# Kernel tuning notes

Hardware: AMD Instinct MI355X
Metric: run time of the kernel (lower is better)

Reference implementation:

```python
import jax, jax.numpy as jnp
import numpy as np

LN_EPS = 1e-5

def _layernorm(x, g, b):
    mu = jnp.mean(x, axis=-1, keepdims=True)
    var = jnp.var(x, axis=-1, keepdims=True)
    return (x - mu) * jax.lax.rsqrt(var + LN_EPS) * g + b

def setup_inputs() -> dict:
    key = jax.random.key(0)
    ks = jax.random.split(key, 8)
    B, N, n, m, a = 4096, 50000, 1024, 16384, 256
    return {
        "x": jax.random.normal(ks[0], (B, n), dtype=jnp.float32),
        "X_data": jax.random.normal(ks[1], (N, n), dtype=jnp.float32),
        "memory_indices": jax.random.randint(ks[2], (m,), 0, N, dtype=jnp.int64)
            if jax.config.jax_enable_x64 else jax.random.randint(ks[2], (m,), 0, N, dtype=jnp.int32),
        "W_q": jax.random.normal(ks[3], (a, n), dtype=jnp.float32) / np.sqrt(n),
        "W_k": jax.random.normal(ks[4], (a, n), dtype=jnp.float32) / np.sqrt(n),
        "W_v": jax.random.normal(ks[5], (n, n), dtype=jnp.float32) / np.sqrt(n),
        "g_q": jnp.ones((a,), jnp.float32), "b_q": jnp.zeros((a,), jnp.float32),
        "g_k": jnp.ones((a,), jnp.float32), "b_k": jnp.zeros((a,), jnp.float32),
        "g_v": jnp.ones((n,), jnp.float32), "b_v": jnp.zeros((n,), jnp.float32),
    }

def reference(x, X_data, memory_indices, W_q, W_k, W_v, g_q, b_q, g_k, b_k, g_v, b_v):
    # Gather memory bank rows: [m, n]
    X_cross = X_data[memory_indices]
    n = x.shape[-1]
    # preprocess(): scalar normalizer so mean row norm ~= sqrt(n) (SAE convention)
    C = jnp.mean(jnp.linalg.norm(X_cross, axis=-1)) / jnp.sqrt(jnp.asarray(n, x.dtype))
    X_cross = X_cross / C
    xs = x / C
    # QKV projections (Linear, no bias) + per-stream LayerNorm
    q = _layernorm(xs @ W_q.T, g_q, b_q)        # [B, a]
    k = _layernorm(X_cross @ W_k.T, g_k, b_k)   # [m, a]
    v = _layernorm(X_cross @ W_v.T, g_v, b_v)   # [m, n]
    # scaled dot-product attention over the memory bank
    scale = 1.0 / np.sqrt(q.shape[-1])
    attn = jax.nn.softmax(jnp.einsum('ba,ma->bm', q, k) * scale, axis=-1)  # [B, m]
    x_hat = attn @ v                             # [B, n]
    return (xs, x_hat, attn, v)
```

## Files before the change

kernel.cpp:

```cpp
#include <hip/hip_runtime.h>
#include <math.h>

typedef _Float16 hlf4 __attribute__((ext_vector_type(4)));
typedef _Float16 hlf8 __attribute__((ext_vector_type(8)));
typedef float f32x4 __attribute__((ext_vector_type(4)));

static __device__ __forceinline__ void gl_lds16(const void* g, void* l) {
    __builtin_amdgcn_global_load_lds(
        (const __attribute__((address_space(1))) unsigned int*)g,
        (__attribute__((address_space(3))) unsigned int*)l, 16, 0, 0);
}

static __device__ __forceinline__ float blk_sum(float v) {
    __shared__ float sm[256];
    int tid = threadIdx.x;
    sm[tid] = v; __syncthreads();
#pragma unroll
    for (int s = 128; s > 0; s >>= 1) {
        if (tid < s) sm[tid] += sm[tid + s];
        __syncthreads();
    }
    float r = sm[0]; __syncthreads();
    return r;
}

static __device__ __forceinline__ float blk_max(float v) {
    __shared__ float sm[256];
    int tid = threadIdx.x;
    sm[tid] = v; __syncthreads();
#pragma unroll
    for (int s = 128; s > 0; s >>= 1) {
        if (tid < s) sm[tid] = fmaxf(sm[tid], sm[tid + s]);
        __syncthreads();
    }
    float r = sm[0]; __syncthreads();
    return r;
}

__global__ __launch_bounds__(256) void k_row_norms(
    const float* __restrict__ X, const int* __restrict__ idx,
    float* __restrict__ norms, int n) {
    long long r = idx[blockIdx.x];
    const float* xr = X + r * (long long)n;
    float s = 0.f;
    for (int k = threadIdx.x * 4; k < n; k += 256 * 4) {
        float4 v = *(const float4*)(xr + k);
        s = fmaf(v.x, v.x, s); s = fmaf(v.y, v.y, s);
        s = fmaf(v.z, v.z, s); s = fmaf(v.w, v.w, s);
    }
    float tot = blk_sum(s);
    if (threadIdx.x == 0) norms[blockIdx.x] = sqrtf(tot);
}

__global__ __launch_bounds__(256) void k_cinv(
    const float* __restrict__ norms, int m, int n, float* __restrict__ cinv) {
    float s = 0.f;
    for (int i = threadIdx.x; i < m; i += 256) s += norms[i];
    float tot = blk_sum(s);
    if (threadIdx.x == 0) cinv[0] = (float)m * sqrtf((float)n) / tot;
}

__global__ __launch_bounds__(256) void k_scale2(
    const float* __restrict__ x, const float* __restrict__ cinv,
    float* __restrict__ y, _Float16* __restrict__ yh, long long total4) {
    float c = cinv[0];
    long long i = blockIdx.x * 256ll + threadIdx.x;
    long long stride = (long long)gridDim.x * 256ll;
    for (; i < total4; i += stride) {
        float4 v = ((const float4*)x)[i];
        v.x *= c; v.y *= c; v.z *= c; v.w *= c;
        ((float4*)y)[i] = v;
        hlf4 o = {(_Float16)v.x, (_Float16)v.y, (_Float16)v.z, (_Float16)v.w};
        ((hlf4*)yh)[i] = o;
    }
}

__global__ __launch_bounds__(256) void k_gather_cvt(
    const float* __restrict__ X, const int* __restrict__ idx,
    const float* __restrict__ cinv, _Float16* __restrict__ out, int n) {
    long long r = idx[blockIdx.x];
    float c = cinv[0];
    const float* src = X + r * (long long)n;
    _Float16* dst = out + (long long)blockIdx.x * n;
    for (int k = threadIdx.x * 4; k < n; k += 256 * 4) {
        float4 v = *(const float4*)(src + k);
        hlf4 o = {(_Float16)(v.x * c), (_Float16)(v.y * c),
                  (_Float16)(v.z * c), (_Float16)(v.w * c)};
        *(hlf4*)(dst + k) = o;
    }
}

__global__ __launch_bounds__(256) void k_cvt(
    const float* __restrict__ in, _Float16* __restrict__ out, long long n4) {
    long long i = blockIdx.x * 256ll + threadIdx.x;
    long long stride = (long long)gridDim.x * 256ll;
    for (; i < n4; i += stride) {
        float4 v = ((const float4*)in)[i];
        hlf4 o = {(_Float16)v.x, (_Float16)v.y, (_Float16)v.z, (_Float16)v.w};
        ((hlf4*)out)[i] = o;
    }
}

__global__ __launch_bounds__(256) void k_tcvt(
    const float* __restrict__ in, _Float16* __restrict__ out, int R, int Cc) {
    __shared__ _Float16 t[32][34];
    int tx = threadIdx.x & 31, ty = threadIdx.x >> 5;
    int c0 = blockIdx.x * 32, r0 = blockIdx.y * 32;
#pragma unroll
    for (int i = 0; i < 32; i += 8)
        t[ty + i][tx] = (_Float16)in[(long long)(r0 + ty + i) * Cc + c0 + tx];
    __syncthreads();
#pragma unroll
    for (int i = 0; i < 32; i += 8)
        out[(long long)(c0 + ty + i) * R + r0 + tx] = t[tx][ty + i];
}

__global__ __launch_bounds__(256) void k_gemm4(
    const _Float16* __restrict__ A, int lda,
    const _Float16* __restrict__ B, int ldb,
    float* __restrict__ Cc, long long ldc, int K,
    float* __restrict__ part, long long zstride) {
    __shared__ _Float16 Ah[2][4096];
    __shared__ _Float16 Bh[2][4096];
    const int tid = threadIdx.x;
    const long long m0 = (long long)blockIdx.x * 128;
    const long long n0 = (long long)blockIdx.y * 128;
    const int KC = K / gridDim.z;
    const int kbase = blockIdx.z * KC;
    const int lane = tid & 63, wv = tid >> 6;
    const int wm = (wv >> 1) * 64, wn = (wv & 1) * 64;
    const int fr = lane & 15, fq = lane >> 4;

    const int s0 = tid, s1 = tid + 256;
    const int r0s = s0 >> 2, r1s = s1 >> 2;
    const int g0 = (((s0 & 3) ^ (r0s & 3)) << 3);
    const int g1 = (((s1 & 3) ^ (r1s & 3)) << 3);
    const _Float16* A0 = A + (m0 + r0s) * (long long)lda + kbase + g0;
    const _Float16* A1 = A + (m0 + r1s) * (long long)lda + kbase + g1;
    const _Float16* B0 = B + (n0 + r0s) * (long long)ldb + kbase + g0;
    const _Float16* B1 = B + (n0 + r1s) * (long long)ldb + kbase + g1;

    f32x4 acc[4][4] = {};

    const int NT = KC / 32;
    {
        gl_lds16(A0, &Ah[0][wv * 512]);
        gl_lds16(A1, &Ah[0][2048 + wv * 512]);
        gl_lds16(B0, &Bh[0][wv * 512]);
        gl_lds16(B1, &Bh[0][2048 + wv * 512]);
    }
    __syncthreads();

    for (int kt = 0; kt < NT; ++kt) {
        const int cur = kt & 1;
        if (kt + 1 < NT) {
            const int nx = cur ^ 1;
            const long long ko = (long long)(kt + 1) * 32;
            gl_lds16(A0 + ko, &Ah[nx][wv * 512]);
            gl_lds16(A1 + ko, &Ah[nx][2048 + wv * 512]);
            gl_lds16(B0 + ko, &Bh[nx][wv * 512]);
            gl_lds16(B1 + ko, &Bh[nx][2048 + wv * 512]);
        }
        hlf8 af[4], bf[4];
#pragma unroll
        for (int i = 0; i < 4; ++i) {
            const int r = wm + i * 16 + fr;
            af[i] = *(const hlf8*)&Ah[cur][r * 32 + ((fq ^ (r & 3)) << 3)];
        }
#pragma unroll
        for (int j = 0; j < 4; ++j) {
            const int r = wn + j * 16 + fr;
            bf[j] = *(const hlf8*)&Bh[cur][r * 32 + ((fq ^ (r & 3)) << 3)];
        }
#pragma unroll
        for (int i = 0; i < 4; ++i)
#pragma unroll
            for (int j = 0; j < 4; ++j)
                acc[i][j] = __builtin_amdgcn_mfma_f32_16x16x32_f16(af[i], bf[j], acc[i][j], 0, 0, 0);
        __syncthreads();
    }

    float* outp = (gridDim.z == 1) ? Cc : (part + (long long)blockIdx.z * zstride);
#pragma unroll
    for (int i = 0; i < 4; ++i)
#pragma unroll
        for (int j = 0; j < 4; ++j) {
            float* cp = outp + (m0 + wm + i * 16 + fq * 4) * ldc + (n0 + wn + j * 16 + fr);
#pragma unroll
            for (int r = 0; r < 4; ++r) cp[(long long)r * ldc] = acc[i][j][r];
        }
}

__global__ __launch_bounds__(512, 2) void k_g256(
    const _Float16* __restrict__ A, int lda,
    const _Float16* __restrict__ B, int ldb,
    float* __restrict__ Cc, long long ldc, int K,
    float* __restrict__ part, long long zstride) {
    __shared__ _Float16 Ah[2][16384];
    __shared__ _Float16 Bh[2][16384];
    const int tid = threadIdx.x, lane = tid & 63, wv = tid >> 6;

    const int gx = gridDim.x, gy = gridDim.y;
    int lin = blockIdx.x + gx * (blockIdx.y + gy * blockIdx.z);
    const int cpx = (gx * gy * (int)gridDim.z) >> 3;
    lin = (lin & 7) * cpx + (lin >> 3);
    const int bx = lin % gx; const int rest = lin / gx;
    const int by = rest % gy, bz = rest / gy;

    const long long m0 = (long long)bx * 256;
    const long long n0 = (long long)by * 256;
    const int KC = K / gridDim.z;
    const int kbase = bz * KC;
    const int wm = (wv >> 2) * 128, wn = (wv & 3) * 64;
    const int fr = lane & 15, fq = lane >> 4;

    const _Float16* srcA[4];
    const _Float16* srcB[4];
#pragma unroll
    for (int j = 0; j < 4; ++j) {
        const int s = j * 512 + tid;
        const int r = s >> 3, p = s & 7;
        const int g = (p ^ (r & 7)) << 3;
        srcA[j] = A + (m0 + r) * (long long)lda + kbase + g;
        srcB[j] = B + (n0 + r) * (long long)ldb + kbase + g;
    }

    f32x4 acc[8][4] = {};

#define ISSUE8(bufi, kt)                                                      \
    {                                                                         \
        const long long ko_ = (long long)(kt) * 64;                           \
        _Float16* la_ = &Ah[bufi][0];                                         \
        _Float16* lb_ = &Bh[bufi][0];                                         \
        gl_lds16(srcA[0] + ko_, la_ + (0 * 512 + wv * 64) * 8);               \
        gl_lds16(srcB[0] + ko_, lb_ + (0 * 512 + wv * 64) * 8);               \
        gl_lds16(srcA[1] + ko_, la_ + (1 * 512 + wv * 64) * 8);               \
        gl_lds16(srcB[1] + ko_, lb_ + (1 * 512 + wv * 64) * 8);               \
        gl_lds16(srcA[2] + ko_, la_ + (2 * 512 + wv * 64) * 8);               \
        gl_lds16(srcB[2] + ko_, lb_ + (2 * 512 + wv * 64) * 8);               \
        gl_lds16(srcA[3] + ko_, la_ + (3 * 512 + wv * 64) * 8);               \
        gl_lds16(srcB[3] + ko_, lb_ + (3 * 512 + wv * 64) * 8);               \
    }

    const int NT = KC / 64;
    ISSUE8(0, 0);
    asm volatile("s_waitcnt vmcnt(0)" ::: "memory");
    __builtin_amdgcn_s_barrier();

    for (int kt = 0; kt < NT; ++kt) {
        const int cur = kt & 1;
        __builtin_amdgcn_s_barrier();
        if (kt + 1 < NT) {
            ISSUE8(cur ^ 1, kt + 1);
            asm volatile("s_waitcnt vmcnt(8)" ::: "memory");
        } else {
            asm volatile("s_waitcnt vmcnt(0)" ::: "memory");
        }
        __builtin_amdgcn_s_barrier();
        __builtin_amdgcn_sched_barrier(0);

        hlf8 af[4][2], bf01[2][2], bf23[2][2];
#pragma unroll
        for (int i = 0; i < 4; ++i)
#pragma unroll
            for (int ks = 0; ks < 2; ++ks) {
                const int rr = wm + i * 16 + fr;
                af[i][ks] = *(const hlf8*)&Ah[cur][rr * 64 + ((((ks * 4 + fq)) ^ (rr & 7)) << 3)];
            }
#pragma unroll
        for (int jj = 0; jj < 2; ++jj)
#pragma unroll
            for (int ks = 0; ks < 2; ++ks) {
                const int cc = wn + jj * 16 + fr;
                bf01[jj][ks] = *(const hlf8*)&Bh[cur][cc * 64 + ((((ks * 4 + fq)) ^ (cc & 7)) << 3)];
            }
        asm volatile("s_waitcnt lgkmcnt(0)" ::: "memory");
        __builtin_amdgcn_sched_barrier(0);
        __builtin_amdgcn_s_setprio(1);
#pragma unroll
        for (int i = 0; i < 4; ++i)
#pragma unroll
            for (int jj = 0; jj < 2; ++jj)
#pragma unroll
                for (int ks = 0; ks < 2; ++ks)
                    acc[i][jj] = __builtin_amdgcn_mfma_f32_16x16x32_f16(af[i][ks], bf01[jj][ks], acc[i][jj], 0, 0, 0);
        __builtin_amdgcn_s_setprio(0);

#pragma unroll
        for (int jj = 0; jj < 2; ++jj)
#pragma unroll
            for (int ks = 0; ks < 2; ++ks) {
                const int cc = wn + (jj + 2) * 16 + fr;
                bf23[jj][ks] = *(const hlf8*)&Bh[cur][cc * 64 + ((((ks * 4 + fq)) ^ (cc & 7)) << 3)];
            }
        asm volatile("s_waitcnt lgkmcnt(0)" ::: "memory");
        __builtin_amdgcn_sched_barrier(0);
        __builtin_amdgcn_s_setprio(1);
#pragma unroll
        for (int i = 0; i < 4; ++i)
#pragma unroll
            for (int jj = 0; jj < 2; ++jj)
#pragma unroll
                for (int ks = 0; ks < 2; ++ks)
                    acc[i][jj + 2] = __builtin_amdgcn_mfma_f32_16x16x32_f16(af[i][ks], bf23[jj][ks], acc[i][jj + 2], 0, 0, 0);
        __builtin_amdgcn_s_setprio(0);

#pragma unroll
        for (int i = 0; i < 4; ++i)
#pragma unroll
            for (int ks = 0; ks < 2; ++ks) {
                const int rr = wm + (i + 4) * 16 + fr;
                af[i][ks] = *(const hlf8*)&Ah[cur][rr * 64 + ((((ks * 4 + fq)) ^ (rr & 7)) << 3)];
            }
        asm volatile("s_waitcnt lgkmcnt(0)" ::: "memory");
        __builtin_amdgcn_sched_barrier(0);
        __builtin_amdgcn_s_setprio(1);
#pragma unroll
        for (int i = 0; i < 4; ++i)
#pragma unroll
            for (int jj = 0; jj < 2; ++jj)
#pragma unroll
                for (int ks = 0; ks < 2; ++ks)
                    acc[i + 4][jj] = __builtin_amdgcn_mfma_f32_16x16x32_f16(af[i][ks], bf01[jj][ks], acc[i + 4][jj], 0, 0, 0);
        __builtin_amdgcn_s_setprio(0);

        __builtin_amdgcn_s_setprio(1);
#pragma unroll
        for (int i = 0; i < 4; ++i)
#pragma unroll
            for (int jj = 0; jj < 2; ++jj)
#pragma unroll
                for (int ks = 0; ks < 2; ++ks)
                    acc[i + 4][jj + 2] = __builtin_amdgcn_mfma_f32_16x16x32_f16(af[i][ks], bf23[jj][ks], acc[i + 4][jj + 2], 0, 0, 0);
        __builtin_amdgcn_s_setprio(0);
    }
#undef ISSUE8

    float* outp = (gridDim.z == 1) ? Cc : (part + (long long)bz * zstride);
#pragma unroll
    for (int i = 0; i < 8; ++i)
#pragma unroll
        for (int j = 0; j < 4; ++j) {
            float* cp = outp + (m0 + wm + i * 16 + fq * 4) * ldc + (n0 + wn + j * 16 + fr);
#pragma unroll
            for (int r = 0; r < 4; ++r) cp[(long long)r * ldc] = acc[i][j][r];
        }
}

__global__ __launch_bounds__(256) void k_redux(
    const float* __restrict__ part, float* __restrict__ out,
    long long n4, long long zs4, int Z) {
    long long i = blockIdx.x * 256ll + threadIdx.x;
    long long stride = (long long)gridDim.x * 256ll;
    for (; i < n4; i += stride) {
        float4 s = ((const float4*)part)[i];
        for (int z = 1; z < Z; ++z) {
            float4 t = ((const float4*)part)[i + z * zs4];
            s.x += t.x; s.y += t.y; s.z += t.z; s.w += t.w;
        }
        ((float4*)out)[i] = s;
    }
}

template <int CNT>
__global__ __launch_bounds__(256) void k_layernorm(
    float* __restrict__ Y, const float* __restrict__ g,
    const float* __restrict__ b, int W) {
    float* yr = Y + (long long)blockIdx.x * W;
    float v[CNT];
    float s = 0.f;
#pragma unroll
    for (int i = 0; i < CNT; ++i) {
        v[i] = yr[threadIdx.x + (i << 8)];
        s += v[i];
    }
    float mu = blk_sum(s) / (float)W;
    float sq = 0.f;
#pragma unroll
    for (int i = 0; i < CNT; ++i) {
        float d = v[i] - mu;
        sq = fmaf(d, d, sq);
    }
    float var = blk_sum(sq) / (float)W;
    float rs = rsqrtf(var + 1e-5f);
#pragma unroll
    for (int i = 0; i < CNT; ++i) {
        int col = threadIdx.x + (i << 8);
        yr[col] = (v[i] - mu) * rs * g[col] + b[col];
    }
}

__global__ __launch_bounds__(256) void k_softmax(
    float* __restrict__ S, _Float16* __restrict__ Sh, float scale) {
    float* sr = S + (long long)blockIdx.x * 16384;
    _Float16* shr = Sh ? Sh + (long long)blockIdx.x * 16384 : nullptr;
    float4 r[16];
    float mx = -1e30f;
#pragma unroll
    for (int i = 0; i < 16; ++i) {
        float4 t = ((const float4*)sr)[threadIdx.x + (i << 8)];
        t.x *= scale; t.y *= scale; t.z *= scale; t.w *= scale;
        r[i] = t;
        mx = fmaxf(mx, fmaxf(fmaxf(t.x, t.y), fmaxf(t.z, t.w)));
    }
    mx = blk_max(mx);
    float sum = 0.f;
#pragma unroll
    for (int i = 0; i < 16; ++i) {
        float4 t = r[i];
        t.x = __expf(t.x - mx); t.y = __expf(t.y - mx);
        t.z = __expf(t.z - mx); t.w = __expf(t.w - mx);
        r[i] = t;
        sum += t.x + t.y + t.z + t.w;
    }
    sum = blk_sum(sum);
    float inv = 1.0f / sum;
#pragma unroll
    for (int i = 0; i < 16; ++i) {
        float4 t = r[i];
        t.x *= inv; t.y *= inv; t.z *= inv; t.w *= inv;
        ((float4*)sr)[threadIdx.x + (i << 8)] = t;
        if (shr) {
            hlf4 o = {(_Float16)t.x, (_Float16)t.y, (_Float16)t.z, (_Float16)t.w};
            ((hlf4*)shr)[threadIdx.x + (i << 8)] = o;
        }
    }
}

extern "C" void kernel_launch(void* const* d_in, const int* in_sizes, int n_in,
                              void* d_out, int out_size, void* d_ws, size_t ws_size,
                              hipStream_t stream) {
    const float* x      = (const float*)d_in[0];
    const float* X_data = (const float*)d_in[1];
    const int*   midx   = (const int*)d_in[2];
    const float* W_q    = (const float*)d_in[3];
    const float* W_k    = (const float*)d_in[4];
    const float* W_v    = (const float*)d_in[5];
    const float* g_q    = (const float*)d_in[6];
    const float* b_q    = (const float*)d_in[7];
    const float* g_k    = (const float*)d_in[8];
    const float* b_k    = (const float*)d_in[9];
    const float* g_v    = (const float*)d_in[10];
    const float* b_v    = (const float*)d_in[11];

    const int n  = in_sizes[10];
    const int a  = in_sizes[6];
    const int m  = in_sizes[2];
    const int Bn = in_sizes[0] / n;

    float* out  = (float*)d_out;
    float* xs   = out;
    float* xhat = xs + (long long)Bn * n;
    float* attn = xhat + (long long)Bn * n;
    float* vout = attn + (long long)Bn * m;

    char* wp = (char*)d_ws;
    auto carve = [&](size_t bytes) -> char* {
        char* r = wp; wp += (bytes + 255) & ~(size_t)255; return r;
    };
    float*     norms = (float*)carve((size_t)m * 4);
    float*     cinv  = (float*)carve(16);
    char*      alias0 = wp;
    float*     qmat  = (float*)carve((size_t)Bn * a * 4);
    float*     kmat  = (float*)carve((size_t)m * a * 4);
    _Float16*  xs_h  = (_Float16*)carve((size_t)Bn * n * 2);
    _Float16*  Xc_h  = (_Float16*)carve((size_t)m * n * 2);
    _Float16*  Wq_h  = (_Float16*)carve((size_t)a * n * 2);
    _Float16*  Wk_h  = (_Float16*)carve((size_t)a * n * 2);
    _Float16*  Wv_h  = (_Float16*)carve((size_t)n * n * 2);
    _Float16*  q_h   = (_Float16*)carve((size_t)Bn * a * 2);
    _Float16*  k_h   = (_Float16*)carve((size_t)m * a * 2);
    float*     splitk = (float*)alias0;
    const int  SK = 4;
    _Float16*  vT_h  = (_Float16*)carve((size_t)n * m * 2);
    size_t used = (size_t)(wp - (char*)d_ws);
    _Float16* attn_h = nullptr;
    if (ws_size >= used + (size_t)Bn * m * 2 + 256)
        attn_h = (_Float16*)carve((size_t)Bn * m * 2);

    hipLaunchKernelGGL(k_row_norms, dim3(m), dim3(256), 0, stream, X_data, midx, norms, n);
    hipLaunchKernelGGL(k_cinv, dim3(1), dim3(256), 0, stream, norms, m, n, cinv);

    hipLaunchKernelGGL(k_scale2, dim3(2048), dim3(256), 0, stream,
                       x, cinv, xs, xs_h, (long long)Bn * n / 4);
    hipLaunchKernelGGL(k_gather_cvt, dim3(m), dim3(256), 0, stream,
                       X_data, midx, cinv, Xc_h, n);

    hipLaunchKernelGGL(k_cvt, dim3(256), dim3(256), 0, stream, W_q, Wq_h, (long long)a * n / 4);
    hipLaunchKernelGGL(k_cvt, dim3(256), dim3(256), 0, stream, W_k, Wk_h, (long long)a * n / 4);
    hipLaunchKernelGGL(k_cvt, dim3(1024), dim3(256), 0, stream, W_v, Wv_h, (long long)n * n / 4);

    hipLaunchKernelGGL(k_gemm4, dim3(Bn / 128, a / 128), dim3(256), 0, stream,
                       xs_h, n, Wq_h, n, qmat, a, n, (float*)nullptr, 0ll);
    hipLaunchKernelGGL(k_gemm4, dim3(m / 128, a / 128), dim3(256), 0, stream,
                       Xc_h, n, Wk_h, n, kmat, a, n, (float*)nullptr, 0ll);
    hipLaunchKernelGGL(k_g256, dim3(m / 256, n / 256), dim3(512), 0, stream,
                       Xc_h, n, Wv_h, n, vout, n, n, (float*)nullptr, 0ll);

    hipLaunchKernelGGL(k_layernorm<1>, dim3(Bn), dim3(256), 0, stream, qmat, g_q, b_q, a);
    hipLaunchKernelGGL(k_layernorm<1>, dim3(m),  dim3(256), 0, stream, kmat, g_k, b_k, a);
    hipLaunchKernelGGL(k_layernorm<4>, dim3(m),  dim3(256), 0, stream, vout, g_v, b_v, n);
    hipLaunchKernelGGL(k_cvt, dim3(1024), dim3(256), 0, stream, qmat, q_h, (long long)Bn * a / 4);
    hipLaunchKernelGGL(k_cvt, dim3(4096), dim3(256), 0, stream, kmat, k_h, (long long)m * a / 4);
    hipLaunchKernelGGL(k_tcvt, dim3(n / 32, m / 32), dim3(256), 0, stream, vout, vT_h, m, n);

    hipLaunchKernelGGL(k_g256, dim3(Bn / 256, m / 256), dim3(512), 0, stream,
                       q_h, a, k_h, a, attn, m, a, (float*)nullptr, 0ll);
    float sc = 1.0f / sqrtf((float)a);
    hipLaunchKernelGGL(k_softmax, dim3(Bn), dim3(256), 0, stream, attn, attn_h, sc);

    long long zstride = (long long)Bn * n;
    if (attn_h) {
        hipLaunchKernelGGL(k_g256, dim3(Bn / 256, n / 256, SK), dim3(512), 0, stream,
                           attn_h, m, vT_h, m, xhat, n, m, splitk, zstride);
    } else {
        hipLaunchKernelGGL(k_g256, dim3(Bn / 256, n / 256, SK), dim3(512), 0, stream,
                           (const _Float16*)attn, m, vT_h, m, xhat, n, m, splitk, zstride);
    }
    hipLaunchKernelGGL(k_redux, dim3(2048), dim3(256), 0, stream,
                       splitk, xhat, (long long)Bn * n / 4, zstride / 4, SK);
}
```

Before: 634.1 us.

## Deepen GEMM prefetch pipeline, emit fp16 scores, fold softmax scale into q

The 256x256 GEMM now keeps two k-tiles in flight. The next-next tile is issued into the freed buffer mid-iteration, and barriers are placed between the LDS-read and MFMA phases instead of a barrier and wait at the loop top. The QK^T GEMM writes fp16 scores directly, with the 1/sqrt(a) scale folded into the q conversion. A new softmax kernel reads those fp16 scores and writes both the fp32 attn and the fp16 copy, which halves the score write/read traffic. Risks are fp16 precision loss on the pre-softmax logits and a rewritten fallback path that converts attn in chunks.

```diff
diff --git a/kernel.cpp b/kernel.cpp
--- a/kernel.cpp
+++ b/kernel.cpp
@@ -91,12 +91,14 @@
 }
 
 __global__ __launch_bounds__(256) void k_cvt(
-    const float* __restrict__ in, _Float16* __restrict__ out, long long n4) {
+    const float* __restrict__ in, _Float16* __restrict__ out, long long n4,
+    float sc) {
     long long i = blockIdx.x * 256ll + threadIdx.x;
     long long stride = (long long)gridDim.x * 256ll;
     for (; i < n4; i += stride) {
         float4 v = ((const float4*)in)[i];
-        hlf4 o = {(_Float16)v.x, (_Float16)v.y, (_Float16)v.z, (_Float16)v.w};
+        hlf4 o = {(_Float16)(v.x * sc), (_Float16)(v.y * sc),
+                  (_Float16)(v.z * sc), (_Float16)(v.w * sc)};
         ((hlf4*)out)[i] = o;
     }
 }
@@ -191,10 +193,11 @@
         }
 }
 
+template <int OUT16>
 __global__ __launch_bounds__(512, 2) void k_g256(
     const _Float16* __restrict__ A, int lda,
     const _Float16* __restrict__ B, int ldb,
-    float* __restrict__ Cc, long long ldc, int K,
+    void* __restrict__ Cc, long long ldc, int K,
     float* __restrict__ part, long long zstride) {
     __shared__ _Float16 Ah[2][16384];
     __shared__ _Float16 Bh[2][16384];
@@ -244,36 +247,30 @@
 
     const int NT = KC / 64;
     ISSUE8(0, 0);
-    asm volatile("s_waitcnt vmcnt(0)" ::: "memory");
-    __builtin_amdgcn_s_barrier();
+    ISSUE8(1, 1);
 
     for (int kt = 0; kt < NT; ++kt) {
         const int cur = kt & 1;
-        __builtin_amdgcn_s_barrier();
-        if (kt + 1 < NT) {
-            ISSUE8(cur ^ 1, kt + 1);
-            asm volatile("s_waitcnt vmcnt(8)" ::: "memory");
-        } else {
-            asm volatile("s_waitcnt vmcnt(0)" ::: "memory");
-        }
-        __builtin_amdgcn_s_barrier();
-        __builtin_amdgcn_sched_barrier(0);
-
-        hlf8 af[4][2], bf01[2][2], bf23[2][2];
+        if (kt + 1 < NT) asm volatile("s_waitcnt vmcnt(8)" ::: "memory");
+        else             asm volatile("s_waitcnt vmcnt(0)" ::: "memory");
+        __builtin_amdgcn_s_barrier();
+
+        hlf8 a0[4][2], a1[4][2], b0[2][2], b1[2][2];
 #pragma unroll
         for (int i = 0; i < 4; ++i)
 #pragma unroll
             for (int ks = 0; ks < 2; ++ks) {
                 const int rr = wm + i * 16 + fr;
-                af[i][ks] = *(const hlf8*)&Ah[cur][rr * 64 + ((((ks * 4 + fq)) ^ (rr & 7)) << 3)];
+                a0[i][ks] = *(const hlf8*)&Ah[cur][rr * 64 + (((ks * 4 + fq) ^ (rr & 7)) << 3)];
             }
 #pragma unroll
         for (int jj = 0; jj < 2; ++jj)
 #pragma unroll
             for (int ks = 0; ks < 2; ++ks) {
                 const int cc = wn + jj * 16 + fr;
-                bf01[jj][ks] = *(const hlf8*)&Bh[cur][cc * 64 + ((((ks * 4 + fq)) ^ (cc & 7)) << 3)];
+                b0[jj][ks] = *(const hlf8*)&Bh[cur][cc * 64 + (((ks * 4 + fq) ^ (cc & 7)) << 3)];
             }
+        __builtin_amdgcn_s_barrier();
         asm volatile("s_waitcnt lgkmcnt(0)" ::: "memory");
         __builtin_amdgcn_sched_barrier(0);
         __builtin_amdgcn_s_setprio(1);
@@ -283,16 +280,18 @@
             for (int jj = 0; jj < 2; ++jj)
 #pragma unroll
                 for (int ks = 0; ks < 2; ++ks)
-                    acc[i][jj] = __builtin_amdgcn_mfma_f32_16x16x32_f16(af[i][ks], bf01[jj][ks], acc[i][jj], 0, 0, 0);
+                    acc[i][jj] = __builtin_amdgcn_mfma_f32_16x16x32_f16(a0[i][ks], b0[jj][ks], acc[i][jj], 0, 0, 0);
         __builtin_amdgcn_s_setprio(0);
+        __builtin_amdgcn_s_barrier();
 
 #pragma unroll
         for (int jj = 0; jj < 2; ++jj)
 #pragma unroll
             for (int ks = 0; ks < 2; ++ks) {
                 const int cc = wn + (jj + 2) * 16 + fr;
-                bf23[jj][ks] = *(const hlf8*)&Bh[cur][cc * 64 + ((((ks * 4 + fq)) ^ (cc & 7)) << 3)];
+                b1[jj][ks] = *(const hlf8*)&Bh[cur][cc * 64 + (((ks * 4 + fq) ^ (cc & 7)) << 3)];
             }
+        __builtin_amdgcn_s_barrier();
         asm volatile("s_waitcnt lgkmcnt(0)" ::: "memory");
         __builtin_amdgcn_sched_barrier(0);
         __builtin_amdgcn_s_setprio(1);
@@ -302,16 +301,18 @@
             for (int jj = 0; jj < 2; ++jj)
 #pragma unroll
                 for (int ks = 0; ks < 2; ++ks)
-                    acc[i][jj + 2] = __builtin_amdgcn_mfma_f32_16x16x32_f16(af[i][ks], bf23[jj][ks], acc[i][jj + 2], 0, 0, 0);
+                    acc[i][jj + 2] = __builtin_amdgcn_mfma_f32_16x16x32_f16(a0[i][ks], b1[jj][ks], acc[i][jj + 2], 0, 0, 0);
         __builtin_amdgcn_s_setprio(0);
+        __builtin_amdgcn_s_barrier();
 
 #pragma unroll
         for (int i = 0; i < 4; ++i)
 #pragma unroll
             for (int ks = 0; ks < 2; ++ks) {
                 const int rr = wm + (i + 4) * 16 + fr;
-                af[i][ks] = *(const hlf8*)&Ah[cur][rr * 64 + ((((ks * 4 + fq)) ^ (rr & 7)) << 3)];
+                a1[i][ks] = *(const hlf8*)&Ah[cur][rr * 64 + (((ks * 4 + fq) ^ (rr & 7)) << 3)];
             }
+        __builtin_amdgcn_s_barrier();
         asm volatile("s_waitcnt lgkmcnt(0)" ::: "memory");
         __builtin_amdgcn_sched_barrier(0);
         __builtin_amdgcn_s_setprio(1);
@@ -321,9 +322,11 @@
             for (int jj = 0; jj < 2; ++jj)
 #pragma unroll
                 for (int ks = 0; ks < 2; ++ks)
-                    acc[i + 4][jj] = __builtin_amdgcn_mfma_f32_16x16x32_f16(af[i][ks], bf01[jj][ks], acc[i + 4][jj], 0, 0, 0);
+                    acc[i + 4][jj] = __builtin_amdgcn_mfma_f32_16x16x32_f16(a1[i][ks], b0[jj][ks], acc[i + 4][jj], 0, 0, 0);
         __builtin_amdgcn_s_setprio(0);
-
+        __builtin_amdgcn_s_barrier();
+
+        if (kt + 2 < NT) ISSUE8(cur, kt + 2);
         __builtin_amdgcn_s_setprio(1);
 #pragma unroll
         for (int i = 0; i < 4; ++i)
@@ -331,20 +334,32 @@
             for (int jj = 0; jj < 2; ++jj)
 #pragma unroll
                 for (int ks = 0; ks < 2; ++ks)
-                    acc[i + 4][jj + 2] = __builtin_amdgcn_mfma_f32_16x16x32_f16(af[i][ks], bf23[jj][ks], acc[i + 4][jj + 2], 0, 0, 0);
+                    acc[i + 4][jj + 2] = __builtin_amdgcn_mfma_f32_16x16x32_f16(a1[i][ks], b1[jj][ks], acc[i + 4][jj + 2], 0, 0, 0);
         __builtin_amdgcn_s_setprio(0);
     }
 #undef ISSUE8
 
-    float* outp = (gridDim.z == 1) ? Cc : (part + (long long)bz * zstride);
-#pragma unroll
-    for (int i = 0; i < 8; ++i)
-#pragma unroll
-        for (int j = 0; j < 4; ++j) {
-            float* cp = outp + (m0 + wm + i * 16 + fq * 4) * ldc + (n0 + wn + j * 16 + fr);
-#pragma unroll
-            for (int r = 0; r < 4; ++r) cp[(long long)r * ldc] = acc[i][j][r];
-        }
+    if constexpr (OUT16) {
+        _Float16* op = (_Float16*)Cc;
+#pragma unroll
+        for (int i = 0; i < 8; ++i)
+#pragma unroll
+            for (int j = 0; j < 4; ++j) {
+                _Float16* cp = op + (m0 + wm + i * 16 + fq * 4) * ldc + (n0 + wn + j * 16 + fr);
+#pragma unroll
+                for (int r = 0; r < 4; ++r) cp[(long long)r * ldc] = (_Float16)acc[i][j][r];
+            }
+    } else {
+        float* outp = (gridDim.z == 1) ? (float*)Cc : (part + (long long)bz * zstride);
+#pragma unroll
+        for (int i = 0; i < 8; ++i)
+#pragma unroll
+            for (int j = 0; j < 4; ++j) {
+                float* cp = outp + (m0 + wm + i * 16 + fq * 4) * ldc + (n0 + wn + j * 16 + fr);
+#pragma unroll
+                for (int r = 0; r < 4; ++r) cp[(long long)r * ldc] = acc[i][j][r];
+            }
+    }
 }
 
 __global__ __launch_bounds__(256) void k_redux(
@@ -387,6 +402,41 @@
     for (int i = 0; i < CNT; ++i) {
         int col = threadIdx.x + (i << 8);
         yr[col] = (v[i] - mu) * rs * g[col] + b[col];
+    }
+}
+
+__global__ __launch_bounds__(256) void k_softmax_h(
+    _Float16* __restrict__ Sh, float* __restrict__ attnf) {
+    _Float16* sr = Sh + (long long)blockIdx.x * 16384;
+    float* ar = attnf + (long long)blockIdx.x * 16384;
+    float4 r[16];
+    float mx = -1e30f;
+#pragma unroll
+    for (int i = 0; i < 16; ++i) {
+        hlf4 h = ((const hlf4*)sr)[threadIdx.x + (i << 8)];
+        float4 t = {(float)h[0], (float)h[1], (float)h[2], (float)h[3]};
+        r[i] = t;
+        mx = fmaxf(mx, fmaxf(fmaxf(t.x, t.y), fmaxf(t.z, t.w)));
+    }
+    mx = blk_max(mx);
+    float sum = 0.f;
+#pragma unroll
+    for (int i = 0; i < 16; ++i) {
+        float4 t = r[i];
+        t.x = __expf(t.x - mx); t.y = __expf(t.y - mx);
+        t.z = __expf(t.z - mx); t.w = __expf(t.w - mx);
+        r[i] = t;
+        sum += t.x + t.y + t.z + t.w;
+    }
+    sum = blk_sum(sum);
+    float inv = 1.0f / sum;
+#pragma unroll
+    for (int i = 0; i < 16; ++i) {
+        float4 t = r[i];
+        t.x *= inv; t.y *= inv; t.z *= inv; t.w *= inv;
+        ((float4*)ar)[threadIdx.x + (i << 8)] = t;
+        hlf4 o = {(_Float16)t.x, (_Float16)t.y, (_Float16)t.z, (_Float16)t.w};
+        ((hlf4*)sr)[threadIdx.x + (i << 8)] = o;
     }
 }
 
@@ -486,37 +536,46 @@
     hipLaunchKernelGGL(k_gather_cvt, dim3(m), dim3(256), 0, stream,
                        X_data, midx, cinv, Xc_h, n);
 
-    hipLaunchKernelGGL(k_cvt, dim3(256), dim3(256), 0, stream, W_q, Wq_h, (long long)a * n / 4);
-    hipLaunchKernelGGL(k_cvt, dim3(256), dim3(256), 0, stream, W_k, Wk_h, (long long)a * n / 4);
-    hipLaunchKernelGGL(k_cvt, dim3(1024), dim3(256), 0, stream, W_v, Wv_h, (long long)n * n / 4);
+    hipLaunchKernelGGL(k_cvt, dim3(256), dim3(256), 0, stream, W_q, Wq_h, (long long)a * n / 4, 1.f);
+    hipLaunchKernelGGL(k_cvt, dim3(256), dim3(256), 0, stream, W_k, Wk_h, (long long)a * n / 4, 1.f);
+    hipLaunchKernelGGL(k_cvt, dim3(1024), dim3(256), 0, stream, W_v, Wv_h, (long long)n * n / 4, 1.f);
 
     hipLaunchKernelGGL(k_gemm4, dim3(Bn / 128, a / 128), dim3(256), 0, stream,
                        xs_h, n, Wq_h, n, qmat, a, n, (float*)nullptr, 0ll);
     hipLaunchKernelGGL(k_gemm4, dim3(m / 128, a / 128), dim3(256), 0, stream,
                        Xc_h, n, Wk_h, n, kmat, a, n, (float*)nullptr, 0ll);
-    hipLaunchKernelGGL(k_g256, dim3(m / 256, n / 256), dim3(512), 0, stream,
+    hipLaunchKernelGGL((k_g256<0>), dim3(m / 256, n / 256), dim3(512), 0, stream,
                        Xc_h, n, Wv_h, n, vout, n, n, (float*)nullptr, 0ll);
 
+    float sc = 1.0f / sqrtf((float)a);
     hipLaunchKernelGGL(k_layernorm<1>, dim3(Bn), dim3(256), 0, stream, qmat, g_q, b_q, a);
     hipLaunchKernelGGL(k_layernorm<1>, dim3(m),  dim3(256), 0, stream, kmat, g_k, b_k, a);
     hipLaunchKernelGGL(k_layernorm<4>, dim3(m),  dim3(256), 0, stream, vout, g_v, b_v, n);
-    hipLaunchKernelGGL(k_cvt, dim3(1024), dim3(256), 0, stream, qmat, q_h, (long long)Bn * a / 4);
-    hipLaunchKernelGGL(k_cvt, dim3(4096), dim3(256), 0, stream, kmat, k_h, (long long)m * a / 4);
+    hipLaunchKernelGGL(k_cvt, dim3(1024), dim3(256), 0, stream, qmat, q_h, (long long)Bn * a / 4, sc);
+    hipLaunchKernelGGL(k_cvt, dim3(4096), dim3(256), 0, stream, kmat, k_h, (long long)m * a / 4, 1.f);
     hipLaunchKernelGGL(k_tcvt, dim3(n / 32, m / 32), dim3(256), 0, stream, vout, vT_h, m, n);
-
-    hipLaunchKernelGGL(k_g256, dim3(Bn / 256, m / 256), dim3(512), 0, stream,
-                       q_h, a, k_h, a, attn, m, a, (float*)nullptr, 0ll);
-    float sc = 1.0f / sqrtf((float)a);
-    hipLaunchKernelGGL(k_softmax, dim3(Bn), dim3(256), 0, stream, attn, attn_h, sc);
 
     long long zstride = (long long)Bn * n;
     if (attn_h) {
-        hipLaunchKernelGGL(k_g256, dim3(Bn / 256, n / 256, SK), dim3(512), 0, stream,
+        hipLaunchKernelGGL((k_g256<1>), dim3(Bn / 256, m / 256), dim3(512), 0, stream,
+                           q_h, a, k_h, a, attn_h, m, a, (float*)nullptr, 0ll);
+        hipLaunchKernelGGL(k_softmax_h, dim3(Bn), dim3(256), 0, stream, attn_h, attn);
+        hipLaunchKernelGGL((k_g256<0>), dim3(Bn / 256, n / 256, SK), dim3(512), 0, stream,
                            attn_h, m, vT_h, m, xhat, n, m, splitk, zstride);
+        hipLaunchKernelGGL(k_redux, dim3(2048), dim3(256), 0, stream,
+                           splitk, xhat, (long long)Bn * n / 4, zstride / 4, SK);
     } else {
-        hipLaunchKernelGGL(k_g256, dim3(Bn / 256, n / 256, SK), dim3(512), 0, stream,
-                           (const _Float16*)attn, m, vT_h, m, xhat, n, m, splitk, zstride);
-    }
-    hipLaunchKernelGGL(k_redux, dim3(2048), dim3(256), 0, stream,
-                       splitk, xhat, (long long)Bn * n / 4, zstride / 4, SK);
-}
+        hipLaunchKernelGGL((k_g256<0>), dim3(Bn / 256, m / 256), dim3(512), 0, stream,
+                           q_h, a, k_h, a, attn, m, a, (float*)nullptr, 0ll);
+        hipLaunchKernelGGL(k_softmax, dim3(Bn), dim3(256), 0, stream, attn, (  _Float16*)nullptr, 1.0f);
+        _Float16* chunk_h = (_Float16*)splitk;
+        for (int cb = 0; cb < 4; ++cb) {
+            const float* src = attn + (long long)cb * 1024 * m;
+            hipLaunchKernelGGL(k_cvt, dim3(4096), dim3(256), 0, stream,
+                               src, chunk_h, (long long)1024 * m / 4, 1.f);
+            hipLaunchKernelGGL((k_g256<0>), dim3(1024 / 256, n / 256), dim3(512), 0, stream,
+                               chunk_h, m, vT_h, m, xhat + (long long)cb * 1024 * n, n, m,
+                               (float*)nullptr, 0ll);
+        }
+    }
+}
```

Result: faster. 614.4 us (-3.1%).
